# Kernel optimization log

Hardware: AMD Instinct MI355X
Metric: run time of the kernel (lower is better)

## Reference

```python
import jax, jax.numpy as jnp
import numpy as np
from jax import lax

B, S, D_MODEL, H, D_CONV, CHUNK = 8, 4096, 1024, 16, 4, 64
D_INNER = D_MODEL


def setup_inputs() -> dict:
    key = jax.random.key(0)
    ks = jax.random.split(key, 6)
    x = jax.random.normal(ks[0], (B, S, D_MODEL), jnp.float32)
    in_proj_w = jax.random.normal(ks[1], (D_INNER + H, D_MODEL), jnp.float32) * 0.02
    conv_w = jax.random.normal(ks[2], (D_INNER, 1, D_CONV), jnp.float32) * 0.3
    conv_b = jnp.zeros((D_INNER,), jnp.float32)
    w_base = jax.random.uniform(ks[3], (H,), jnp.float32, minval=-0.5, maxval=0.5)
    out_proj_w = jax.random.normal(ks[4], (D_MODEL, D_INNER), jnp.float32) * 0.02
    return {"x": x, "in_proj_w": in_proj_w, "conv_w": conv_w, "conv_b": conv_b,
            "w_base": w_base, "out_proj_w": out_proj_w}


def _segsum(a):
    # a: (..., T) -> (..., T, T) with out[i, j] = sum_{k=j+1..i} a[k] for i>=j else -inf
    T = a.shape[-1]
    lower_strict = jnp.tril(jnp.ones((T, T), bool), -1)   # row i > col j
    lower = jnp.tril(jnp.ones((T, T), bool), 0)
    xr = jnp.where(lower_strict, a[..., :, None], 0.0)    # (..., T, T)
    s = jnp.cumsum(xr, axis=-2)
    return jnp.where(lower, s, -jnp.inf)


def _ssd(x, A, l):
    # x: (b, s, h, n); A: (b, s, h); l = chunk size
    b, s, h, n = x.shape
    c = s // l
    x = x.reshape(b, c, l, h, n)
    A = A.reshape(b, c, l, h).transpose(0, 3, 1, 2)        # (b, h, c, l)
    A_cumsum = jnp.cumsum(A, axis=-1)

    # intra-chunk (diagonal) part
    L_log = _segsum(A)                                      # (b, h, c, l, l)
    L = jnp.exp(L_log - jnp.max(L_log, axis=-1, keepdims=True))
    norm_diag = L.sum(-1).transpose(0, 2, 3, 1)             # (b, c, l, h)
    Y_diag = jnp.einsum('bhcls,bcshn->bclhn', L, x)

    # chunk states
    decay_states = A_cumsum[..., -1:] - A_cumsum            # (b, h, c, l)
    decay_states = jnp.exp(decay_states - jnp.max(decay_states, axis=-1, keepdims=True))
    norm_decay = decay_states.sum(-1).transpose(0, 2, 1)    # (b, c, h)
    states = jnp.einsum('bhcl,bclhn->bchn', decay_states, x)

    norm_decay = jnp.pad(norm_decay, ((0, 0), (1, 0), (0, 0)))
    states = jnp.pad(states, ((0, 0), (1, 0), (0, 0), (0, 0)))

    # inter-chunk recurrence
    decay_chunk = _segsum(jnp.pad(A_cumsum[..., -1], ((0, 0), (0, 0), (1, 0))))  # (b,h,c+1,c+1)
    decay_chunk = jnp.exp(decay_chunk - jnp.max(decay_chunk, axis=-1, keepdims=True))
    norm_decay = jnp.einsum('bhzc,bch->bzh', decay_chunk, norm_decay)[:, :-1]    # (b, c, h)
    states = jnp.einsum('bhzc,bchn->bzhn', decay_chunk, states)[:, :-1]          # (b, c, h, n)

    # off-diagonal output
    state_decay_out = jnp.exp(A_cumsum - jnp.max(A_cumsum, axis=-1, keepdims=True))
    norm_off = jnp.einsum('bch,bhcl->bclh', norm_decay, state_decay_out)
    Y_off = jnp.einsum('bchn,bhcl->bclhn', states, state_decay_out)

    Y = (Y_diag + Y_off).reshape(b, s, h, n)
    norm = (norm_diag + norm_off).reshape(b, s, h)
    return Y / norm[..., None]


def reference(x, in_proj_w, conv_w, conv_b, w_base, out_proj_w):
    b, s, d_model = x.shape
    d_inner = in_proj_w.shape[0] - H
    xw = jnp.einsum('bsd,ed->bse', x, in_proj_w)            # (b, s, d_inner + H)
    xi, w = xw[..., :d_inner], xw[..., d_inner:]            # (b,s,d_inner), (b,s,H)
    # causal depthwise conv (padding k-1 on the left == pad both + slice [:s])
    xc = lax.conv_general_dilated(
        xi.transpose(0, 2, 1), conv_w, window_strides=(1,),
        padding=[(D_CONV - 1, 0)], feature_group_count=d_inner,
        dimension_numbers=('NCH', 'OIH', 'NCH'))
    xc = (xc + conv_b[None, :, None]).transpose(0, 2, 1)    # (b, s, d_inner)
    xh = xc.reshape(b, s, H, d_inner // H)                  # (b, s, h, n)
    A = w * w_base                                          # (b, s, H)
    y = _ssd(xh, A, CHUNK)                                  # (b, s, h, n)
    y = y.reshape(b, s, d_inner)
    return jnp.einsum('bsd,ed->bse', y, out_proj_w)         # (b, s, d_model)
```

## Files before the change

### kernel.cpp

```cpp
#include <hip/hip_runtime.h>
#include <hip/hip_bf16.h>
#include <cstdint>

#define B_ 8
#define S_ 4096
#define DM 1024
#define H_ 16
#define DN 64
#define CH 64
#define NC 64
#define M_ (B_ * S_)

typedef unsigned short u16;
typedef u16 u16x8 __attribute__((ext_vector_type(8)));
typedef u16 u16x4 __attribute__((ext_vector_type(4)));
typedef float f32x4 __attribute__((ext_vector_type(4)));
typedef __bf16 bf16x8 __attribute__((ext_vector_type(8)));

__device__ __forceinline__ float bf2f(u16 u) { return __uint_as_float(((unsigned)u) << 16); }
__device__ __forceinline__ u16 f2bf(float f) { __bf16 h = (__bf16)f; return __builtin_bit_cast(u16, h); }

#define GLOAD16(gp, lp) \
  __builtin_amdgcn_global_load_lds((__attribute__((address_space(1))) const void*)(gp), \
                                   (__attribute__((address_space(3))) void*)(lp), 16, 0, 0)
#define BAR()   asm volatile("s_barrier" ::: "memory")
#define VMCNT4() asm volatile("s_waitcnt vmcnt(4)" ::: "memory")
#define VMCNT0() asm volatile("s_waitcnt vmcnt(0)" ::: "memory")

__device__ __forceinline__ void stage_unit(const u16* __restrict__ src, int row0, int kt,
                                           int ks, u16* ldsu, int t, int K) {
#pragma unroll
  for (int i = 0; i < 2; ++i) {
    int f = i * 512 + t;
    int row = f >> 2, j = f & 3;
    int g = j ^ ((row >> 1) & 3);
    GLOAD16(src + (size_t)(row0 + row) * K + kt * 64 + ks * 32 + g * 8, ldsu + f * 8);
  }
}

__device__ __forceinline__ void lda4(bf16x8* fr, const u16* unit, int rbase, int lr, int lk) {
#pragma unroll
  for (int q = 0; q < 4; ++q) {
    int row = rbase + q * 16 + lr;
    int cell = row * 4 + (lk ^ ((row >> 1) & 3));
    fr[q] = *reinterpret_cast<const bf16x8*>(&unit[cell * 8]);
  }
}

__device__ __forceinline__ void mfma16(f32x4 (&acc)[8][4], int mh, const bf16x8* aF, const bf16x8* bF) {
  __builtin_amdgcn_s_setprio(1);
#pragma unroll
  for (int q = 0; q < 4; ++q)
#pragma unroll
    for (int nf = 0; nf < 4; ++nf)
      acc[mh * 4 + q][nf] = __builtin_amdgcn_mfma_f32_16x16x32_bf16(aF[q], bF[nf], acc[mh * 4 + q][nf], 0, 0, 0);
  __builtin_amdgcn_s_setprio(0);
}

template<int MODE>
__global__ __launch_bounds__(512, 2) void bgemm8(
    const u16* __restrict__ A, const u16* __restrict__ Bw,
    void* __restrict__ Cout, int K)
{
  __shared__ u16 lds[8][8192];
  const int orig = blockIdx.x;
  const int swz  = (orig & 7) * 64 + (orig >> 3);
  const int m0 = (swz >> 2) * 256;
  const int n0 = (swz & 3) * 256;
  const int t  = threadIdx.x;
  const int wid = t >> 6, l = t & 63;
  const int wm = wid >> 2, wn = wid & 3;
  const int lr = l & 15, lk = l >> 4;
  const int arb = wm * 128;
  const int brb = wn * 64;

  f32x4 acc[8][4];
#pragma unroll
  for (int i = 0; i < 8; ++i)
#pragma unroll
    for (int j = 0; j < 4; ++j) acc[i][j] = (f32x4){0.f, 0.f, 0.f, 0.f};

  stage_unit(A,  m0, 0, 0, lds[0], t, K);
  stage_unit(Bw, n0, 0, 0, lds[2], t, K);
  stage_unit(A,  m0, 0, 1, lds[1], t, K);
  stage_unit(Bw, n0, 0, 1, lds[3], t, K);
  stage_unit(Bw, n0, 1, 0, lds[6], t, K);
  stage_unit(Bw, n0, 1, 1, lds[7], t, K);
  VMCNT4();
  BAR();

  bf16x8 aF[4], bF0[4], bF1[4];
  for (int i = 0; i < 8; ++i) {
    const bool st = (i < 7);
    lda4(aF, lds[0], arb, lr, lk);
    lda4(bF0, lds[2], brb, lr, lk);
    stage_unit(A, m0, 2 * i + 1, 0, lds[4], t, K);
    BAR(); mfma16(acc, 0, aF, bF0);
    lda4(aF, lds[1], arb, lr, lk);
    lda4(bF1, lds[3], brb, lr, lk);
    stage_unit(A, m0, 2 * i + 1, 1, lds[5], t, K);
    BAR(); mfma16(acc, 0, aF, bF1);
    lda4(aF, lds[0], arb + 64, lr, lk);
    if (st) stage_unit(Bw, n0, 2 * i + 2, 0, lds[2], t, K);
    BAR(); mfma16(acc, 1, aF, bF0);
    lda4(aF, lds[1], arb + 64, lr, lk);
    if (st) stage_unit(Bw, n0, 2 * i + 2, 1, lds[3], t, K);
    if (st) VMCNT4(); else VMCNT0();
    BAR(); mfma16(acc, 1, aF, bF1);
    lda4(aF, lds[4], arb, lr, lk);
    lda4(bF0, lds[6], brb, lr, lk);
    if (st) stage_unit(A, m0, 2 * i + 2, 0, lds[0], t, K);
    BAR(); mfma16(acc, 0, aF, bF0);
    lda4(aF, lds[5], arb, lr, lk);
    lda4(bF1, lds[7], brb, lr, lk);
    if (st) stage_unit(A, m0, 2 * i + 2, 1, lds[1], t, K);
    BAR(); mfma16(acc, 0, aF, bF1);
    lda4(aF, lds[4], arb + 64, lr, lk);
    if (st) stage_unit(Bw, n0, 2 * i + 3, 0, lds[6], t, K);
    BAR(); mfma16(acc, 1, aF, bF0);
    lda4(aF, lds[5], arb + 64, lr, lk);
    if (st) stage_unit(Bw, n0, 2 * i + 3, 1, lds[7], t, K);
    if (st) VMCNT4();
    BAR(); mfma16(acc, 1, aF, bF1);
  }

#pragma unroll
  for (int mf = 0; mf < 8; ++mf) {
#pragma unroll
    for (int nf = 0; nf < 4; ++nf) {
      int n  = n0 + wn * 64 + nf * 16 + lr;
      int mb = m0 + wm * 128 + mf * 16 + lk * 4;
#pragma unroll
      for (int r = 0; r < 4; ++r) {
        if (MODE == 0) ((float*)Cout)[(size_t)(mb + r) * 1024 + n] = acc[mf][nf][r];
        else           ((u16*)Cout)[(size_t)(mb + r) * 1024 + n] = f2bf(acc[mf][nf][r]);
      }
    }
  }
}

__global__ __launch_bounds__(256) void prep_kernel(
    const float* __restrict__ ipw, const float* __restrict__ opw,
    u16* __restrict__ wbf_in, u16* __restrict__ wbf_out, u16* __restrict__ wlo)
{
  int b = blockIdx.x;
  if (b < 1032) {
    const float* src = (b < 520) ? ipw : opw;
    u16* dst = (b < 520) ? wbf_in : wbf_out;
    size_t i = ((size_t)(b < 520 ? b : b - 520) * 256 + threadIdx.x) * 8;
    f32x4 a = *reinterpret_cast<const f32x4*>(&src[i]);
    f32x4 c = *reinterpret_cast<const f32x4*>(&src[i + 4]);
    u16x8 o;
#pragma unroll
    for (int j = 0; j < 4; ++j) { o[j] = f2bf(a[j]); o[4 + j] = f2bf(c[j]); }
    *reinterpret_cast<u16x8*>(&dst[i]) = o;
  } else {
    size_t e = ((size_t)(b - 1032) * 256 + threadIdx.x) * 8;
    f32x4 a = *reinterpret_cast<const f32x4*>(&ipw[1048576 + e]);
    f32x4 c = *reinterpret_cast<const f32x4*>(&ipw[1048576 + e + 4]);
    u16x8 o;
#pragma unroll
    for (int j = 0; j < 4; ++j) {
      u16 h = f2bf(a[j]); o[j]     = f2bf(a[j] - bf2f(h));
      u16 g = f2bf(c[j]); o[4 + j] = f2bf(c[j] - bf2f(g));
    }
    *reinterpret_cast<u16x8*>(&wlo[e]) = o;
  }
}

__global__ __launch_bounds__(256) void wsplit(
    const float* __restrict__ x, const u16* __restrict__ wbf, const u16* __restrict__ wlo,
    u16* __restrict__ xbf, float* __restrict__ wbufT)
{
  __shared__ u16 hi[4][16 * 5 * 8];
  __shared__ u16 lo[4][16 * 5 * 8];
  __shared__ float comb[3][64][4];
  const int t = threadIdx.x;
  const int w = t >> 6, l = t & 63;
  const int r0 = blockIdx.x * 16;
  const int k0 = w * 256;
  const int lr = l & 15, lk = l >> 4;
  const int srow = l >> 2, skc = l & 3;
  u16* HI = hi[w];
  u16* LO = lo[w];

  const float* gx  = &x[(size_t)(r0 + srow) * 1024 + k0 + skc * 8];
  const u16*   gbh = &wbf[(size_t)(1024 + lr) * 1024 + k0 + lk * 8];
  const u16*   gbl = &wlo[(size_t)lr * 1024 + k0 + lk * 8];

  f32x4 a0 = *reinterpret_cast<const f32x4*>(gx);
  f32x4 a1 = *reinterpret_cast<const f32x4*>(gx + 4);
  bf16x8 bh = *reinterpret_cast<const bf16x8*>(gbh);
  bf16x8 bl = *reinterpret_cast<const bf16x8*>(gbl);

  f32x4 acc = (f32x4){0.f, 0.f, 0.f, 0.f};
  const int wcell = srow * 5 + skc;
  const int rcell = lr * 5 + lk;

  for (int kt = 0; kt < 8; ++kt) {
    f32x4 n0, n1; bf16x8 nbh, nbl;
    if (kt < 7) {
      n0  = *reinterpret_cast<const f32x4*>(gx + (kt + 1) * 32);
      n1  = *reinterpret_cast<const f32x4*>(gx + (kt + 1) * 32 + 4);
      nbh = *reinterpret_cast<const bf16x8*>(gbh + (kt + 1) * 32);
      nbl = *reinterpret_cast<const bf16x8*>(gbl + (kt + 1) * 32);
    }
    u16x8 h8, l8;
#pragma unroll
    for (int j = 0; j < 4; ++j) {
      u16 ha = f2bf(a0[j]); h8[j]     = ha; l8[j]     = f2bf(a0[j] - bf2f(ha));
      u16 hb = f2bf(a1[j]); h8[4 + j] = hb; l8[4 + j] = f2bf(a1[j] - bf2f(hb));
    }
    *reinterpret_cast<u16x8*>(&xbf[(size_t)(r0 + srow) * 1024 + k0 + kt * 32 + skc * 8]) = h8;
    *reinterpret_cast<u16x8*>(&HI[wcell * 8]) = h8;
    *reinterpret_cast<u16x8*>(&LO[wcell * 8]) = l8;
    asm volatile("s_waitcnt lgkmcnt(0)" ::: "memory");
    __builtin_amdgcn_sched_barrier(0);
    bf16x8 ah = *reinterpret_cast<const bf16x8*>(&HI[rcell * 8]);
    bf16x8 al = *reinterpret_cast<const bf16x8*>(&LO[rcell * 8]);
    acc = __builtin_amdgcn_mfma_f32_16x16x32_bf16(ah, bh, acc, 0, 0, 0);
    acc = __builtin_amdgcn_mfma_f32_16x16x32_bf16(al, bh, acc, 0, 0, 0);
    acc = __builtin_amdgcn_mfma_f32_16x16x32_bf16(ah, bl, acc, 0, 0, 0);
    a0 = n0; a1 = n1; bh = nbh; bl = nbl;
  }
  if (w) {
#pragma unroll
    for (int r = 0; r < 4; ++r) comb[w - 1][l][r] = acc[r];
  }
  __syncthreads();
  if (!w) {
#pragma unroll
    for (int r = 0; r < 4; ++r) acc[r] += comb[0][l][r] + comb[1][l][r] + comb[2][l][r];
    *reinterpret_cast<f32x4*>(&wbufT[(size_t)lr * M_ + r0 + lk * 4]) = acc;
  }
}

__global__ __launch_bounds__(256) void chunk_kernel(
    const u16* __restrict__ xi,
    const float* __restrict__ cw, const float* __restrict__ cb,
    const float* __restrict__ wbufT, const float* __restrict__ w_base,
    u16* __restrict__ ybuf, float* __restrict__ Acum, float* __restrict__ acbuf,
    float* __restrict__ normd, float* __restrict__ states, float* __restrict__ ndbuf)
{
  int bi = blockIdx.x;
  int c  = bi & 63;
  int h  = (bi >> 6) & 15;
  int b  = bi >> 10;
  int bh = b * 16 + h;
  int t  = threadIdx.x;
  __shared__ u16 xis[67][64];
  __shared__ u16 xsT[64][66];
  __shared__ float pc[CH], m1s[CH], dsv[CH];
  __shared__ float wls[4][64];
  __shared__ float cbs[64];
  size_t m0 = (size_t)b * S_ + (size_t)c * CH;
  size_t abase = ((size_t)bh * NC + c) * CH;

  wls[t & 3][t >> 2] = cw[(size_t)h * 256 + t];
  if (t < 64) cbs[t] = cb[h * 64 + t];

  {
    int g8  = t & 7;
    int hr0 = t >> 3;
    for (int hr = hr0; hr < 67; hr += 32) {
      u16x8 v = {0, 0, 0, 0, 0, 0, 0, 0};
      if (!(c == 0 && hr < 3))
        v = *reinterpret_cast<const u16x8*>(&xi[(m0 - 3 + hr) * DM + h * 64 + g8 * 8]);
      *reinterpret_cast<u16x8*>(&xis[hr][g8 * 8]) = v;
    }
  }

  if (t < 64) {
    float p = wbufT[(size_t)h * M_ + m0 + t] * w_base[h];
#pragma unroll
    for (int off = 1; off < 64; off <<= 1) {
      float v = __shfl_up(p, off);
      if (t >= off) p += v;
    }
    Acum[abase + t] = p;
    if (t == 63) acbuf[(size_t)bh * NC + c] = p;
    pc[t] = p;
    float rmin = p;
#pragma unroll
    for (int off = 1; off < 64; off <<= 1) {
      float v = __shfl_up(rmin, off);
      if (t >= off) rmin = fminf(rmin, v);
    }
    m1s[t] = p - rmin;
    float minall = __shfl(rmin, 63);
    dsv[t] = __expf(minall - p);
  }
  __syncthreads();

  {
    int n  = t & 63;
    int lb = (t >> 6) * 16;
    float w0 = wls[0][n], w1 = wls[1][n], w2 = wls[2][n], w3 = wls[3][n];
    float bias = cbs[n];
    float a = bf2f(xis[lb + 0][n]);
    float bv = bf2f(xis[lb + 1][n]);
    float cv = bf2f(xis[lb + 2][n]);
    u16x8 o0, o1;
#pragma unroll
    for (int r = 0; r < 16; ++r) {
      float dv = bf2f(xis[lb + r + 3][n]);
      float s = fmaf(w3, dv, fmaf(w2, cv, fmaf(w1, bv, fmaf(w0, a, bias))));
      if (r < 8) o0[r] = f2bf(s); else o1[r - 8] = f2bf(s);
      a = bv; bv = cv; cv = dv;
    }
    *reinterpret_cast<u16x8*>(&xsT[n][lb]) = o0;
    *reinterpret_cast<u16x8*>(&xsT[n][lb + 8]) = o1;
  }
  __syncthreads();

  {
    int w = t >> 6, l = t & 63;
    int lr = l & 15, lk = l >> 4;
    int row = w * 16 + lr;
    float pr = pc[row], m1r = m1s[row];
    bf16x8 afr[2];
    float np = 0.f;
#pragma unroll
    for (int ks = 0; ks < 2; ++ks) {
      int sbase = ks * 32 + lk * 8;
      u16x8 av;
#pragma unroll
      for (int j = 0; j < 8; ++j) {
        int s = sbase + j;
        float L = (s <= row) ? __expf(pr - pc[s] - m1r) : 0.f;
        np += L;
        av[j] = f2bf(L);
      }
      afr[ks] = __builtin_bit_cast(bf16x8, av);
    }
    np += __shfl_xor(np, 16);
    np += __shfl_xor(np, 32);
    if (lk == 0) normd[abase + row] = np;

    f32x4 acc[4];
#pragma unroll
    for (int nf = 0; nf < 4; ++nf) acc[nf] = (f32x4){0.f, 0.f, 0.f, 0.f};
#pragma unroll
    for (int ks = 0; ks < 2; ++ks)
#pragma unroll
      for (int nf = 0; nf < 4; ++nf) {
        bf16x8 bfr = *reinterpret_cast<const bf16x8*>(&xsT[nf * 16 + lr][ks * 32 + lk * 8]);
        acc[nf] = __builtin_amdgcn_mfma_f32_16x16x32_bf16(afr[ks], bfr, acc[nf], 0, 0, 0);
      }
#pragma unroll
    for (int nf = 0; nf < 4; ++nf)
#pragma unroll
      for (int r = 0; r < 4; ++r)
        ybuf[(m0 + w * 16 + lk * 4 + r) * DM + h * 64 + nf * 16 + lr] = f2bf(acc[nf][r]);
  }

  if (t < 64) {
    float acc = 0.f;
#pragma unroll
    for (int l8 = 0; l8 < 64; l8 += 8) {
      u16x8 xv = *reinterpret_cast<const u16x8*>(&xsT[t][l8]);
#pragma unroll
      for (int j = 0; j < 8; ++j) acc = fmaf(dsv[l8 + j], bf2f(xv[j]), acc);
    }
    states[((size_t)bh * NC + c) * DN + t] = acc;
    float v = dsv[t];
#pragma unroll
    for (int off = 32; off >= 1; off >>= 1) v += __shfl_down(v, off);
    if (t == 0) ndbuf[(size_t)bh * NC + c] = v;
  }
}

__global__ __launch_bounds__(256) void interchunk_kernel(
    const float* __restrict__ acbuf, const float* __restrict__ states,
    const float* __restrict__ ndbuf, float* __restrict__ nstates, float* __restrict__ nndbuf)
{
  int bh = blockIdx.x;
  int t  = threadIdx.x;
  __shared__ float Ssum[NC], minP[NC], ndl[NC];
  if (t < 64) {
    float ac = acbuf[(size_t)bh * NC + t];
    float S = ac;
#pragma unroll
    for (int off = 1; off < 64; off <<= 1) {
      float v = __shfl_up(S, off);
      if (t >= off) S += v;
    }
    float Pc = S - ac;
    float mp = Pc;
#pragma unroll
    for (int off = 1; off < 64; off <<= 1) {
      float v = __shfl_up(mp, off);
      if (t >= off) mp = fminf(mp, v);
    }
    Ssum[t] = S;
    minP[t] = mp;
    ndl[t]  = ndbuf[(size_t)bh * NC + t];
  }
  __syncthreads();
  int n  = t & 63;
  int r0 = t >> 6;
  for (int r = 0; r < 16; ++r) {
    int z = r0 + r * 4;
    float mpz = minP[z];
    float acc = 0.f;
    for (int j = 0; j < z; ++j) {
      float e = __expf(mpz - Ssum[j]);
      acc = fmaf(e, states[((size_t)bh * NC + j) * DN + n], acc);
    }
    nstates[((size_t)bh * NC + z) * DN + n] = acc;
  }
  if (t < 64) {
    int z = t;
    float mpz = minP[z];
    float acc = 0.f;
    for (int j = 0; j < z; ++j) acc = fmaf(__expf(mpz - Ssum[j]), ndl[j], acc);
    nndbuf[(size_t)bh * NC + z] = acc;
  }
}

__global__ __launch_bounds__(256) void final_kernel(
    const float* __restrict__ Acum, const float* __restrict__ normd,
    const float* __restrict__ nstates, const float* __restrict__ nndbuf,
    u16* __restrict__ ybuf)
{
  int bi = blockIdx.x;
  int c  = bi & 63;
  int h  = (bi >> 6) & 15;
  int b  = bi >> 10;
  int bh = b * 16 + h;
  int t  = threadIdx.x;
  __shared__ float sdo[CH], nrm[CH], sto[DN];
  __shared__ float ndo_s;
  size_t abase = ((size_t)bh * NC + c) * CH;
  if (t < 64) {
    float p = Acum[abase + t];
    float m3 = p;
#pragma unroll
    for (int off = 32; off >= 1; off >>= 1) m3 = fmaxf(m3, __shfl_down(m3, off));
    m3 = __shfl(m3, 0);
    sdo[t] = __expf(p - m3);
    nrm[t] = normd[abase + t];
    sto[t] = nstates[((size_t)bh * NC + c) * DN + t];
    if (t == 0) ndo_s = nndbuf[(size_t)bh * NC + c];
  }
  __syncthreads();
  size_t m0 = (size_t)b * S_ + (size_t)c * CH;
  int g  = t & 7;
  int l0 = t >> 3;
  float ndo = ndo_s;
  for (int li = l0; li < 64; li += 32) {
    size_t a = (m0 + li) * DM + h * DN + g * 8;
    u16x8 v = *reinterpret_cast<u16x8*>(&ybuf[a]);
    float sd = sdo[li];
    float rec = 1.f / (nrm[li] + ndo * sd);
    u16x8 o;
#pragma unroll
    for (int jj = 0; jj < 8; ++jj) {
      float yd = bf2f(v[jj]);
      o[jj] = f2bf((yd + sto[g * 8 + jj] * sd) * rec);
    }
    *reinterpret_cast<u16x8*>(&ybuf[a]) = o;
  }
}

extern "C" void kernel_launch(void* const* d_in, const int* in_sizes, int n_in,
                              void* d_out, int out_size, void* d_ws, size_t ws_size,
                              hipStream_t stream) {
  const float* x          = (const float*)d_in[0];
  const float* in_proj_w  = (const float*)d_in[1];
  const float* conv_w     = (const float*)d_in[2];
  const float* conv_b     = (const float*)d_in[3];
  const float* w_base     = (const float*)d_in[4];
  const float* out_proj_w = (const float*)d_in[5];
  float* out = (float*)d_out;
  char* ws = (char*)d_ws;

  u16*   wbf_in  = (u16*)  (ws + 0);
  u16*   wbf_out = (u16*)  (ws + 2129920);
  u16*   wlo16   = (u16*)  (ws + 4227072);
  float* wbufT   = (float*)(ws + 4259840);
  float* Acum    = (float*)(ws + 6356992);
  float* acbuf   = (float*)(ws + 8454144);
  float* normd   = (float*)(ws + 8486912);
  float* states  = (float*)(ws + 10584064);
  float* ndbuf   = (float*)(ws + 12681216);
  float* nstates = (float*)(ws + 12713984);
  float* nndbuf  = (float*)(ws + 14811136);
  u16*   xbf     = (u16*)  (ws + 14843904);
  u16*   xibf    = (u16*)  (ws + 81952768);
  u16*   ybuf    = xbf;

  prep_kernel<<<1040, 256, 0, stream>>>(in_proj_w, out_proj_w, wbf_in, wbf_out, wlo16);
  wsplit<<<2048, 256, 0, stream>>>(x, wbf_in, wlo16, xbf, wbufT);
  bgemm8<1><<<512, 512, 0, stream>>>(xbf, wbf_in, (void*)xibf, DM);
  chunk_kernel<<<8192, 256, 0, stream>>>(xibf, conv_w, conv_b, wbufT, w_base,
                                         ybuf, Acum, acbuf, normd, states, ndbuf);
  interchunk_kernel<<<128, 256, 0, stream>>>(acbuf, states, ndbuf, nstates, nndbuf);
  final_kernel<<<8192, 256, 0, stream>>>(Acum, normd, nstates, nndbuf, ybuf);
  bgemm8<0><<<512, 512, 0, stream>>>(ybuf, wbf_out, (void*)out, DM);
}
```

Before: 282.3 us.

## Move intra-chunk diagonal compute into final kernel, recomputing conv to skip ybuf round trip

```diff
diff --git a/kernel.cpp b/kernel.cpp
--- a/kernel.cpp
+++ b/kernel.cpp
@@ -235,12 +235,11 @@
   }
 }
 
-__global__ __launch_bounds__(256) void chunk_kernel(
-    const u16* __restrict__ xi,
-    const float* __restrict__ cw, const float* __restrict__ cb,
+__global__ __launch_bounds__(256) void statesk(
+    const u16* __restrict__ xi, const float* __restrict__ cw, const float* __restrict__ cb,
     const float* __restrict__ wbufT, const float* __restrict__ w_base,
-    u16* __restrict__ ybuf, float* __restrict__ Acum, float* __restrict__ acbuf,
-    float* __restrict__ normd, float* __restrict__ states, float* __restrict__ ndbuf)
+    float* __restrict__ Acum, float* __restrict__ acbuf,
+    float* __restrict__ states, float* __restrict__ ndbuf)
 {
   int bi = blockIdx.x;
   int c  = bi & 63;
@@ -250,7 +249,7 @@
   int t  = threadIdx.x;
   __shared__ u16 xis[67][64];
   __shared__ u16 xsT[64][66];
-  __shared__ float pc[CH], m1s[CH], dsv[CH];
+  __shared__ float dsv[CH];
   __shared__ float wls[4][64];
   __shared__ float cbs[64];
   size_t m0 = (size_t)b * S_ + (size_t)c * CH;
@@ -279,14 +278,12 @@
     }
     Acum[abase + t] = p;
     if (t == 63) acbuf[(size_t)bh * NC + c] = p;
-    pc[t] = p;
     float rmin = p;
 #pragma unroll
     for (int off = 1; off < 64; off <<= 1) {
       float v = __shfl_up(rmin, off);
       if (t >= off) rmin = fminf(rmin, v);
     }
-    m1s[t] = p - rmin;
     float minall = __shfl(rmin, 63);
     dsv[t] = __expf(minall - p);
   }
@@ -312,47 +309,6 @@
     *reinterpret_cast<u16x8*>(&xsT[n][lb + 8]) = o1;
   }
   __syncthreads();
-
-  {
-    int w = t >> 6, l = t & 63;
-    int lr = l & 15, lk = l >> 4;
-    int row = w * 16 + lr;
-    float pr = pc[row], m1r = m1s[row];
-    bf16x8 afr[2];
-    float np = 0.f;
-#pragma unroll
-    for (int ks = 0; ks < 2; ++ks) {
-      int sbase = ks * 32 + lk * 8;
-      u16x8 av;
-#pragma unroll
-      for (int j = 0; j < 8; ++j) {
-        int s = sbase + j;
-        float L = (s <= row) ? __expf(pr - pc[s] - m1r) : 0.f;
-        np += L;
-        av[j] = f2bf(L);
-      }
-      afr[ks] = __builtin_bit_cast(bf16x8, av);
-    }
-    np += __shfl_xor(np, 16);
-    np += __shfl_xor(np, 32);
-    if (lk == 0) normd[abase + row] = np;
-
-    f32x4 acc[4];
-#pragma unroll
-    for (int nf = 0; nf < 4; ++nf) acc[nf] = (f32x4){0.f, 0.f, 0.f, 0.f};
-#pragma unroll
-    for (int ks = 0; ks < 2; ++ks)
-#pragma unroll
-      for (int nf = 0; nf < 4; ++nf) {
-        bf16x8 bfr = *reinterpret_cast<const bf16x8*>(&xsT[nf * 16 + lr][ks * 32 + lk * 8]);
-        acc[nf] = __builtin_amdgcn_mfma_f32_16x16x32_bf16(afr[ks], bfr, acc[nf], 0, 0, 0);
-      }
-#pragma unroll
-    for (int nf = 0; nf < 4; ++nf)
-#pragma unroll
-      for (int r = 0; r < 4; ++r)
-        ybuf[(m0 + w * 16 + lk * 4 + r) * DM + h * 64 + nf * 16 + lr] = f2bf(acc[nf][r]);
-  }
 
   if (t < 64) {
     float acc = 0.f;
@@ -418,10 +374,10 @@
   }
 }
 
-__global__ __launch_bounds__(256) void final_kernel(
-    const float* __restrict__ Acum, const float* __restrict__ normd,
-    const float* __restrict__ nstates, const float* __restrict__ nndbuf,
-    u16* __restrict__ ybuf)
+__global__ __launch_bounds__(256) void finalsY(
+    const u16* __restrict__ xi, const float* __restrict__ cw, const float* __restrict__ cb,
+    const float* __restrict__ Acum, const float* __restrict__ nstates,
+    const float* __restrict__ nndbuf, u16* __restrict__ ybuf)
 {
   int bi = blockIdx.x;
   int c  = bi & 63;
@@ -429,37 +385,116 @@
   int b  = bi >> 10;
   int bh = b * 16 + h;
   int t  = threadIdx.x;
-  __shared__ float sdo[CH], nrm[CH], sto[DN];
+  __shared__ u16 xis[67][64];
+  __shared__ u16 xsT[64][66];
+  __shared__ float pc[CH], m1s[CH], sdo_s[CH], sto_s[DN], nrm_s[CH];
+  __shared__ float wls[4][64];
+  __shared__ float cbs[64];
   __shared__ float ndo_s;
+  size_t m0 = (size_t)b * S_ + (size_t)c * CH;
   size_t abase = ((size_t)bh * NC + c) * CH;
+
+  wls[t & 3][t >> 2] = cw[(size_t)h * 256 + t];
+  if (t < 64) cbs[t] = cb[h * 64 + t];
+
+  {
+    int g8  = t & 7;
+    int hr0 = t >> 3;
+    for (int hr = hr0; hr < 67; hr += 32) {
+      u16x8 v = {0, 0, 0, 0, 0, 0, 0, 0};
+      if (!(c == 0 && hr < 3))
+        v = *reinterpret_cast<const u16x8*>(&xi[(m0 - 3 + hr) * DM + h * 64 + g8 * 8]);
+      *reinterpret_cast<u16x8*>(&xis[hr][g8 * 8]) = v;
+    }
+  }
+
   if (t < 64) {
     float p = Acum[abase + t];
+    pc[t] = p;
+    float rmin = p;
+#pragma unroll
+    for (int off = 1; off < 64; off <<= 1) {
+      float v = __shfl_up(rmin, off);
+      if (t >= off) rmin = fminf(rmin, v);
+    }
+    m1s[t] = p - rmin;
     float m3 = p;
 #pragma unroll
     for (int off = 32; off >= 1; off >>= 1) m3 = fmaxf(m3, __shfl_down(m3, off));
     m3 = __shfl(m3, 0);
-    sdo[t] = __expf(p - m3);
-    nrm[t] = normd[abase + t];
-    sto[t] = nstates[((size_t)bh * NC + c) * DN + t];
+    sdo_s[t] = __expf(p - m3);
+    sto_s[t] = nstates[((size_t)bh * NC + c) * DN + t];
     if (t == 0) ndo_s = nndbuf[(size_t)bh * NC + c];
   }
   __syncthreads();
-  size_t m0 = (size_t)b * S_ + (size_t)c * CH;
-  int g  = t & 7;
-  int l0 = t >> 3;
-  float ndo = ndo_s;
-  for (int li = l0; li < 64; li += 32) {
-    size_t a = (m0 + li) * DM + h * DN + g * 8;
-    u16x8 v = *reinterpret_cast<u16x8*>(&ybuf[a]);
-    float sd = sdo[li];
-    float rec = 1.f / (nrm[li] + ndo * sd);
-    u16x8 o;
-#pragma unroll
-    for (int jj = 0; jj < 8; ++jj) {
-      float yd = bf2f(v[jj]);
-      o[jj] = f2bf((yd + sto[g * 8 + jj] * sd) * rec);
-    }
-    *reinterpret_cast<u16x8*>(&ybuf[a]) = o;
+
+  {
+    int n  = t & 63;
+    int lb = (t >> 6) * 16;
+    float w0 = wls[0][n], w1 = wls[1][n], w2 = wls[2][n], w3 = wls[3][n];
+    float bias = cbs[n];
+    float a = bf2f(xis[lb + 0][n]);
+    float bv = bf2f(xis[lb + 1][n]);
+    float cv = bf2f(xis[lb + 2][n]);
+    u16x8 o0, o1;
+#pragma unroll
+    for (int r = 0; r < 16; ++r) {
+      float dv = bf2f(xis[lb + r + 3][n]);
+      float s = fmaf(w3, dv, fmaf(w2, cv, fmaf(w1, bv, fmaf(w0, a, bias))));
+      if (r < 8) o0[r] = f2bf(s); else o1[r - 8] = f2bf(s);
+      a = bv; bv = cv; cv = dv;
+    }
+    *reinterpret_cast<u16x8*>(&xsT[n][lb]) = o0;
+    *reinterpret_cast<u16x8*>(&xsT[n][lb + 8]) = o1;
+  }
+  __syncthreads();
+
+  {
+    int w = t >> 6, l = t & 63;
+    int lr = l & 15, lk = l >> 4;
+    int row = w * 16 + lr;
+    float pr = pc[row], m1r = m1s[row];
+    bf16x8 afr[2];
+    float np = 0.f;
+#pragma unroll
+    for (int ks = 0; ks < 2; ++ks) {
+      int sbase = ks * 32 + lk * 8;
+      u16x8 av;
+#pragma unroll
+      for (int j = 0; j < 8; ++j) {
+        int s = sbase + j;
+        float L = (s <= row) ? __expf(pr - pc[s] - m1r) : 0.f;
+        np += L;
+        av[j] = f2bf(L);
+      }
+      afr[ks] = __builtin_bit_cast(bf16x8, av);
+    }
+    np += __shfl_xor(np, 16);
+    np += __shfl_xor(np, 32);
+    if (lk == 0) nrm_s[row] = np;
+
+    f32x4 acc[4];
+#pragma unroll
+    for (int nf = 0; nf < 4; ++nf) acc[nf] = (f32x4){0.f, 0.f, 0.f, 0.f};
+#pragma unroll
+    for (int ks = 0; ks < 2; ++ks)
+#pragma unroll
+      for (int nf = 0; nf < 4; ++nf) {
+        bf16x8 bfr = *reinterpret_cast<const bf16x8*>(&xsT[nf * 16 + lr][ks * 32 + lk * 8]);
+        acc[nf] = __builtin_amdgcn_mfma_f32_16x16x32_bf16(afr[ks], bfr, acc[nf], 0, 0, 0);
+      }
+    __syncthreads();
+    float ndo = ndo_s;
+#pragma unroll
+    for (int nf = 0; nf < 4; ++nf)
+#pragma unroll
+      for (int r = 0; r < 4; ++r) {
+        int orow = w * 16 + lk * 4 + r;
+        float sd = sdo_s[orow];
+        float rec = 1.f / (nrm_s[orow] + ndo * sd);
+        float yv = (acc[nf][r] + sto_s[nf * 16 + lr] * sd) * rec;
+        ybuf[(m0 + orow) * DM + h * 64 + nf * 16 + lr] = f2bf(yv);
+      }
   }
 }
 
@@ -481,7 +516,6 @@
   float* wbufT   = (float*)(ws + 4259840);
   float* Acum    = (float*)(ws + 6356992);
   float* acbuf   = (float*)(ws + 8454144);
-  float* normd   = (float*)(ws + 8486912);
   float* states  = (float*)(ws + 10584064);
   float* ndbuf   = (float*)(ws + 12681216);
   float* nstates = (float*)(ws + 12713984);
@@ -493,9 +527,9 @@
   prep_kernel<<<1040, 256, 0, stream>>>(in_proj_w, out_proj_w, wbf_in, wbf_out, wlo16);
   wsplit<<<2048, 256, 0, stream>>>(x, wbf_in, wlo16, xbf, wbufT);
   bgemm8<1><<<512, 512, 0, stream>>>(xbf, wbf_in, (void*)xibf, DM);
-  chunk_kernel<<<8192, 256, 0, stream>>>(xibf, conv_w, conv_b, wbufT, w_base,
-                                         ybuf, Acum, acbuf, normd, states, ndbuf);
+  statesk<<<8192, 256, 0, stream>>>(xibf, conv_w, conv_b, wbufT, w_base,
+                                    Acum, acbuf, states, ndbuf);
   interchunk_kernel<<<128, 256, 0, stream>>>(acbuf, states, ndbuf, nstates, nndbuf);
-  final_kernel<<<8192, 256, 0, stream>>>(Acum, normd, nstates, nndbuf, ybuf);
+  finalsY<<<8192, 256, 0, stream>>>(xibf, conv_w, conv_b, Acum, nstates, nndbuf, ybuf);
   bgemm8<0><<<512, 512, 0, stream>>>(ybuf, wbf_out, (void*)out, DM);
 }
```

New measurement: 283.4 us (median of 2 runs). Within noise of the previous version (+0.4%).
